# Performance work log

Measured on AMD Instinct MI355X. Metric: run time of the kernel, lower is better.

The kernel has to match this reference:

```python
import jax, jax.numpy as jnp
import numpy as np

D = 768      # d_model (hardcoded in module)
H = 12       # heads (ViT-Base)
HD = D // H  # head_dim = 64
FF = 4 * D   # mlp hidden = 3072
L = 32       # num_latents
B, N = 64, 197
EPS = 1e-6


def _ln(x, g, b):
    mu = jnp.mean(x, axis=-1, keepdims=True)
    var = jnp.mean(jnp.square(x - mu), axis=-1, keepdims=True)
    return (x - mu) * jax.lax.rsqrt(var + EPS) * g + b


def _attn_simple(q, k, v):
    # fusion attention: single-head, scale = C ** -0.5 over full dim
    C = q.shape[-1]
    a = jax.nn.softmax(jnp.einsum('bnc,bmc->bnm', q, k) * (C ** -0.5), axis=-1)
    return jnp.einsum('bnm,bmc->bnc', a, v)


def _mha(x, qkv_w, qkv_b, proj_w, proj_b):
    Bx, Nx, C = x.shape
    qkv = (x @ qkv_w + qkv_b).reshape(Bx, Nx, 3, H, HD)
    q, k, v = jnp.moveaxis(qkv, 2, 0)           # each [B, N, H, HD]
    scores = jnp.einsum('bnhd,bmhd->bhnm', q, k) * (HD ** -0.5)
    a = jax.nn.softmax(scores, axis=-1)
    out = jnp.einsum('bhnm,bmhd->bnhd', a, v).reshape(Bx, Nx, C)
    return out @ proj_w + proj_b


def _mlp(x, w1, b1, w2, b2):
    return jax.nn.gelu(x @ w1 + b1, approximate=False) @ w2 + b2


def setup_inputs() -> dict:
    key = jax.random.key(0)
    ks = iter(jax.random.split(key, 40))
    std = 0.02
    d = {
        'x': jax.random.normal(next(ks), (B, N, D), jnp.float32),
        'y': jax.random.normal(next(ks), (B, N, D), jnp.float32),
        'latents': jax.random.normal(next(ks), (1, L, D), jnp.float32) * std,
        'scale_a': jnp.zeros((1,), jnp.float32) + 0.1,
        'scale_v': jnp.zeros((1,), jnp.float32) + 0.1,
    }
    for p in ('p', 'm'):
        d[f'{p}_n1_g'] = jnp.ones((D,), jnp.float32)
        d[f'{p}_n1_b'] = jnp.zeros((D,), jnp.float32)
        d[f'{p}_qkv_w'] = jax.random.normal(next(ks), (D, 3 * D), jnp.float32) * std
        d[f'{p}_qkv_b'] = jnp.zeros((3 * D,), jnp.float32)
        d[f'{p}_proj_w'] = jax.random.normal(next(ks), (D, D), jnp.float32) * std
        d[f'{p}_proj_b'] = jnp.zeros((D,), jnp.float32)
        d[f'{p}_n2_g'] = jnp.ones((D,), jnp.float32)
        d[f'{p}_n2_b'] = jnp.zeros((D,), jnp.float32)
        d[f'{p}_fc1_w'] = jax.random.normal(next(ks), (D, FF), jnp.float32) * std
        d[f'{p}_fc1_b'] = jnp.zeros((FF,), jnp.float32)
        d[f'{p}_fc2_w'] = jax.random.normal(next(ks), (FF, D), jnp.float32) * std
        d[f'{p}_fc2_b'] = jnp.zeros((D,), jnp.float32)
    return d


def reference(x, y, latents, scale_a, scale_v,
              p_n1_g, p_n1_b, p_qkv_w, p_qkv_b, p_proj_w, p_proj_b,
              p_n2_g, p_n2_b, p_fc1_w, p_fc1_b, p_fc2_w, p_fc2_b,
              m_n1_g, m_n1_b, m_qkv_w, m_qkv_b, m_proj_w, m_proj_b,
              m_n2_g, m_n2_b, m_fc1_w, m_fc1_b, m_fc2_w, m_fc2_b):
    BS = x.shape[0]
    # ---- fusion: latent bottleneck cross-attention ----
    concat = jnp.concatenate([x, y], axis=1)                       # [B, 2N, D]
    lat = jnp.broadcast_to(latents, (BS, L, D))
    fused = _attn_simple(lat, concat, concat)                      # [B, L, D]
    x = x + scale_a * _attn_simple(x, fused, fused)
    y = y + scale_v * _attn_simple(y, fused, fused)
    # ---- pre-norm attn + MLP blocks ----
    x = x + _mha(_ln(x, p_n1_g, p_n1_b), p_qkv_w, p_qkv_b, p_proj_w, p_proj_b)
    y = y + _mha(_ln(y, m_n1_g, m_n1_b), m_qkv_w, m_qkv_b, m_proj_w, m_proj_b)
    x = x + _mlp(_ln(x, p_n2_g, p_n2_b), p_fc1_w, p_fc1_b, p_fc2_w, p_fc2_b)
    y = y + _mlp(_ln(y, m_n2_g, m_n2_b), m_fc1_w, m_fc1_b, m_fc2_w, m_fc2_b)
    return (x, y)
```

## Files before the change

kernel.cpp:

```cpp
#include <hip/hip_runtime.h>
#include <math.h>


namespace {

constexpr int BB = 64, NN = 197, DD = 768, HH = 12, HDIM = 64, FF = 3072, LL = 32;
constexpr int N2 = 2 * NN;
constexpr int ROWS = BB * NN;
constexpr float SCALE_D = 0.036084391824351615f;
constexpr float SCALE_H = 0.125f;

constexpr long long B_AHI    = 0;
constexpr long long B_ALO    = 19365888;
constexpr long long B_GHI    = 40894464;
constexpr long long B_GLO    = 118358016;
constexpr long long B_CONCAT = 0;
constexpr long long B_SCORES = 0;
constexpr long long B_QKV    = 125829120;
constexpr long long B_FUSED  = 242221056;
constexpr long long B_S1T    = 248512512;
constexpr long long B_A2     = 252706816;
constexpr long long B_S2     = 256901120;
constexpr long long B_PHI    = 258998272;
constexpr long long B_PLO    = 278364160;
constexpr long long B_WHI    = 297795584;
constexpr long long B_WLO    = 303038464;

__device__ inline ushort f2bf(float f) {
  unsigned x = __float_as_uint(f);
  unsigned r = (x + 0x7FFFu + ((x >> 16) & 1u)) >> 16;
  return (ushort)r;
}
__device__ inline float bf2f(ushort u) {
  return __uint_as_float(((unsigned)u) << 16);
}

using bf16x8v = __attribute__((ext_vector_type(8))) short;
using f32x4v  = __attribute__((ext_vector_type(4))) float;

enum { ME_BIAS = 0, ME_RESID_BIAS = 1, ME_GELU_SPLIT = 2 };

struct MP {
  const ushort* Ah; const ushort* Al; int lda;
  const ushort* Wh; const ushort* Wl; int ldw;
  float* C; int ldc;
  const float* bias;
  const float* R; int ldr;
  ushort* Oh; ushort* Ol; int ldo;
  int M, N, K;
  int nxb, nwg;
};

template <int EPI>
__global__ __launch_bounds__(256, 3) void mgemm_k(MP p) {
  __shared__ ushort sAh[128 * 32], sAl[128 * 32], sBh[128 * 32], sBl[128 * 32];
  const int tid = threadIdx.x;

  const int nwg = p.nwg;
  const int h = blockIdx.x;
  const int q = nwg >> 3, r = nwg & 7;
  const int xcd = h & 7, ii = h >> 3;
  const int wg = (xcd < r ? xcd * (q + 1) : r * (q + 1) + (xcd - r) * q) + ii;
  const int m0 = (wg / p.nxb) * 128;
  const int n0 = (wg % p.nxb) * 128;

  const int l = tid & 63, w = tid >> 6;
  const int wm = (w >> 1) * 64, wn = (w & 1) * 64;
  const int fr = l & 15, fq = l >> 4;

  ushort* const lbuf = (w == 0) ? sAh : (w == 1) ? sAl : (w == 2) ? sBh : sBl;
  const ushort* const gsrc = (w == 0) ? p.Ah : (w == 1) ? p.Al
                            : (w == 2) ? p.Wh : p.Wl;
  const int ldg   = (w < 2) ? p.lda : p.ldw;
  const int rbase = (w < 2) ? m0 : n0;
  const int rlim  = ((w < 2) ? p.M : p.N) - 1;
  const int rl = l >> 2;
  const int ch = l & 3;

  f32x4v acc[4][4];
#pragma unroll
  for (int i = 0; i < 4; ++i)
#pragma unroll
    for (int j = 0; j < 4; ++j)
#pragma unroll
      for (int t = 0; t < 4; ++t) acc[i][j][t] = 0.f;

  for (int k0 = 0; k0 < p.K; k0 += 32) {
#pragma unroll
    for (int j = 0; j < 8; ++j) {
      int rg = rbase + j * 16 + rl;
      rg = rg > rlim ? rlim : rg;
      const ushort* gp = gsrc + (long long)rg * ldg + k0 + ch * 8;
      __builtin_amdgcn_global_load_lds(
          (const __attribute__((address_space(1))) void*)gp,
          (__attribute__((address_space(3))) void*)(lbuf + j * 512),
          16, 0, 0);
    }
    __syncthreads();

    bf16x8v ah[4], al[4];
#pragma unroll
    for (int mi = 0; mi < 4; ++mi) {
      const int ro = (wm + mi * 16 + fr) * 32 + fq * 8;
      ah[mi] = *reinterpret_cast<const bf16x8v*>(&sAh[ro]);
      al[mi] = *reinterpret_cast<const bf16x8v*>(&sAl[ro]);
    }
#pragma unroll
    for (int ni = 0; ni < 4; ++ni) {
      const int ro = (wn + ni * 16 + fr) * 32 + fq * 8;
      const bf16x8v bh = *reinterpret_cast<const bf16x8v*>(&sBh[ro]);
      const bf16x8v bl = *reinterpret_cast<const bf16x8v*>(&sBl[ro]);
#pragma unroll
      for (int mi = 0; mi < 4; ++mi) {
        acc[mi][ni] = __builtin_amdgcn_mfma_f32_16x16x32_bf16(al[mi], bh, acc[mi][ni], 0, 0, 0);
        acc[mi][ni] = __builtin_amdgcn_mfma_f32_16x16x32_bf16(ah[mi], bl, acc[mi][ni], 0, 0, 0);
        acc[mi][ni] = __builtin_amdgcn_mfma_f32_16x16x32_bf16(ah[mi], bh, acc[mi][ni], 0, 0, 0);
      }
    }
    __syncthreads();
  }

#pragma unroll
  for (int mi = 0; mi < 4; ++mi) {
    const int rb = m0 + wm + mi * 16 + fq * 4;
#pragma unroll
    for (int ni = 0; ni < 4; ++ni) {
      const int col = n0 + wn + ni * 16 + fr;
#pragma unroll
      for (int t = 0; t < 4; ++t) {
        const int mg = rb + t;
        if (mg >= p.M) continue;
        float v = acc[mi][ni][t];
        if (EPI == ME_BIAS) {
          p.C[(long long)mg * p.ldc + col] = v + p.bias[col];
        } else if (EPI == ME_RESID_BIAS) {
          p.C[(long long)mg * p.ldc + col] =
              v + p.bias[col] + p.R[(long long)mg * p.ldr + col];
        } else {
          v += p.bias[col];
          v = 0.5f * v * (1.f + erff(v * 0.70710678118654752f));
          const ushort hh = f2bf(v);
          const long long o = (long long)mg * p.ldo + col;
          p.Oh[o] = hh;
          p.Ol[o] = f2bf(v - bf2f(hh));
        }
      }
    }
  }
}

template <int EPI>
static void launch_mgemm(hipStream_t st, MP p) {
  p.nxb = p.N / 128;
  p.nwg = p.nxb * ((p.M + 127) / 128);
  hipLaunchKernelGGL(HIP_KERNEL_NAME(mgemm_k<EPI>), dim3(p.nwg), dim3(256), 0, st, p);
}

struct GemmP {
  const float* A; long long sA1, sA2; int lda;
  const float* W; long long sW1, sW2; int ldw;
  float*       C; long long sC1, sC2; int ldc;
  const float* R; long long sR1, sR2; int ldr;
  const float* bias;
  const float* scaleptr;
  ushort* Oh; ushort* Ol;
  int M, N, K, Z2;
  float alpha;
};

enum { E_NONE = 0, E_BIAS = 1, E_RESID_SCALE = 4, E_SPLIT = 5 };

template <int BM, int BN, int BK, int TM, int TN, bool WT, int EPI>
__global__ __launch_bounds__(256) void gemm_k(GemmP p) {
  constexpr int NX = BN / TN;
  __shared__ float As[BK][BM + 4];
  __shared__ float Ws[BK][BN + 4];

  const int tid = threadIdx.x;
  const int z = blockIdx.z;
  const int z1 = z / p.Z2, z2 = z % p.Z2;
  const float* A = p.A + (long long)z1 * p.sA1 + (long long)z2 * p.sA2;
  const float* W = p.W + (long long)z1 * p.sW1 + (long long)z2 * p.sW2;
  float*       C = p.C ? p.C + (long long)z1 * p.sC1 + (long long)z2 * p.sC2 : nullptr;
  const float* R = p.R ? p.R + (long long)z1 * p.sR1 + (long long)z2 * p.sR2 : nullptr;
  ushort* Oh = p.Oh ? p.Oh + (long long)z1 * p.sC1 + (long long)z2 * p.sC2 : nullptr;
  ushort* Ol = p.Ol ? p.Ol + (long long)z1 * p.sC1 + (long long)z2 * p.sC2 : nullptr;

  const int m0 = blockIdx.y * BM;
  const int n0 = blockIdx.x * BN;
  const int tx = tid % NX;
  const int ty = tid / NX;

  float acc[TM][TN];
#pragma unroll
  for (int i = 0; i < TM; ++i)
#pragma unroll
    for (int j = 0; j < TN; ++j) acc[i][j] = 0.f;

  for (int k0 = 0; k0 < p.K; k0 += BK) {
    for (int l = tid; l < BM * BK; l += 256) {
      const int m = l / BK, kc = l % BK;
      const int mg = m0 + m, kg = k0 + kc;
      float v = 0.f;
      if (mg < p.M && kg < p.K) v = A[(long long)mg * p.lda + kg];
      As[kc][m] = v;
    }
    if (!WT) {
      for (int l = tid; l < BK * BN; l += 256) {
        const int kc = l / BN, n = l % BN;
        const int ng = n0 + n, kg = k0 + kc;
        float v = 0.f;
        if (ng < p.N && kg < p.K) v = W[(long long)kg * p.ldw + ng];
        Ws[kc][n] = v;
      }
    } else {
      for (int l = tid; l < BK * BN; l += 256) {
        const int n = l / BK, kc = l % BK;
        const int ng = n0 + n, kg = k0 + kc;
        float v = 0.f;
        if (ng < p.N && kg < p.K) v = W[(long long)ng * p.ldw + kg];
        Ws[kc][n] = v;
      }
    }
    __syncthreads();

#pragma unroll
    for (int kk = 0; kk < BK; ++kk) {
      float af[TM], wf[TN];
#pragma unroll
      for (int i = 0; i < TM; i += 4) {
        const float4 t = *reinterpret_cast<const float4*>(&As[kk][ty * TM + i]);
        af[i] = t.x; af[i + 1] = t.y; af[i + 2] = t.z; af[i + 3] = t.w;
      }
#pragma unroll
      for (int j = 0; j < TN; j += 4) {
        const float4 t = *reinterpret_cast<const float4*>(&Ws[kk][tx * TN + j]);
        wf[j] = t.x; wf[j + 1] = t.y; wf[j + 2] = t.z; wf[j + 3] = t.w;
      }
#pragma unroll
      for (int i = 0; i < TM; ++i)
#pragma unroll
        for (int j = 0; j < TN; ++j) acc[i][j] += af[i] * wf[j];
    }
    __syncthreads();
  }

  float sc = 0.f;
  if (EPI == E_RESID_SCALE) sc = p.scaleptr[0];
#pragma unroll
  for (int i = 0; i < TM; ++i) {
    const int mg = m0 + ty * TM + i;
    if (mg >= p.M) continue;
#pragma unroll
    for (int j = 0; j < TN; ++j) {
      const int ng = n0 + tx * TN + j;
      if (ng >= p.N) continue;
      float v = acc[i][j];
      if (EPI == E_NONE) v *= p.alpha;
      if (EPI == E_BIAS) v += p.bias[ng];
      if (EPI == E_RESID_SCALE) v = R[(long long)mg * p.ldr + ng] + sc * v;
      if (EPI == E_SPLIT) {
        const long long o = (long long)mg * p.ldc + ng;
        const ushort hh = f2bf(v);
        Oh[o] = hh;
        Ol[o] = f2bf(v - bf2f(hh));
      } else {
        C[(long long)mg * p.ldc + ng] = v;
      }
    }
  }
}

template <int BM, int BN, int BK, int TM, int TN, bool WT, int EPI>
static void launch_gemm(hipStream_t st, const GemmP& p, int Z) {
  dim3 grid((p.N + BN - 1) / BN, (p.M + BM - 1) / BM, Z);
  hipLaunchKernelGGL(HIP_KERNEL_NAME(gemm_k<BM, BN, BK, TM, TN, WT, EPI>),
                     grid, dim3(256), 0, st, p);
}


__global__ __launch_bounds__(256) void concat_k(const float* __restrict__ x,
                                                const float* __restrict__ y,
                                                float* __restrict__ c) {
  const long long total4 = (long long)BB * N2 * DD / 4;
  const long long i = (long long)blockIdx.x * 256 + threadIdx.x;
  if (i >= total4) return;
  const long long e = i * 4;
  const int b = (int)(e / ((long long)N2 * DD));
  const long long rem = e % ((long long)N2 * DD);
  const int r = (int)(rem / DD);
  const int col = (int)(rem % DD);
  const float* src = (r < NN) ? (x + ((long long)b * NN + r) * DD + col)
                              : (y + ((long long)b * NN + (r - NN)) * DD + col);
  reinterpret_cast<float4*>(c)[i] = *reinterpret_cast<const float4*>(src);
}

__global__ __launch_bounds__(256) void ln_split_k(const float* __restrict__ in,
                                                  ushort* __restrict__ oh,
                                                  ushort* __restrict__ ol,
                                                  const float* __restrict__ g,
                                                  const float* __restrict__ b) {
  const int row = blockIdx.x;
  const int tid = threadIdx.x;
  const float* src = in + (long long)row * DD;
  const float v0 = src[tid], v1 = src[tid + 256], v2 = src[tid + 512];
  __shared__ float red[4];
  const int wid = tid >> 6;

  float s = v0 + v1 + v2;
#pragma unroll
  for (int o = 32; o; o >>= 1) s += __shfl_xor(s, o);
  if ((tid & 63) == 0) red[wid] = s;
  __syncthreads();
  const float mu = (red[0] + red[1] + red[2] + red[3]) * (1.f / 768.f);
  const float d0 = v0 - mu, d1 = v1 - mu, d2 = v2 - mu;
  __syncthreads();

  float qv = d0 * d0 + d1 * d1 + d2 * d2;
#pragma unroll
  for (int o = 32; o; o >>= 1) qv += __shfl_xor(qv, o);
  if ((tid & 63) == 0) red[wid] = qv;
  __syncthreads();
  const float var = (red[0] + red[1] + red[2] + red[3]) * (1.f / 768.f);
  const float rs = 1.f / sqrtf(var + 1e-6f);

  ushort* dh = oh + (long long)row * DD;
  ushort* dl = ol + (long long)row * DD;
#pragma unroll
  for (int c = 0; c < 3; ++c) {
    const int idx = tid + c * 256;
    const float dv = (c == 0 ? d0 : c == 1 ? d1 : d2);
    const float v = dv * rs * g[idx] + b[idx];
    const ushort hh = f2bf(v);
    dh[idx] = hh;
    dl[idx] = f2bf(v - bf2f(hh));
  }
}

__global__ __launch_bounds__(256) void wsplit_k(const float* __restrict__ W,
                                                ushort* __restrict__ th,
                                                ushort* __restrict__ tl,
                                                int K, int N) {
  __shared__ float t[32][33];
  const int tid = threadIdx.x;
  const int kb = blockIdx.y * 32, nb = blockIdx.x * 32;
  for (int u = tid; u < 1024; u += 256) {
    const int k = u >> 5, n = u & 31;
    t[k][n] = W[(long long)(kb + k) * N + nb + n];
  }
  __syncthreads();
  const int n = tid >> 3, k4 = tid & 7;
  ushort4 vh, vl;
  {
    float v;
    v = t[k4 * 4 + 0][n]; vh.x = f2bf(v); vl.x = f2bf(v - bf2f(vh.x));
    v = t[k4 * 4 + 1][n]; vh.y = f2bf(v); vl.y = f2bf(v - bf2f(vh.y));
    v = t[k4 * 4 + 2][n]; vh.z = f2bf(v); vl.z = f2bf(v - bf2f(vh.z));
    v = t[k4 * 4 + 3][n]; vh.w = f2bf(v); vl.w = f2bf(v - bf2f(vh.w));
  }
  const long long o = (long long)(nb + n) * K + kb + k4 * 4;
  *reinterpret_cast<ushort4*>(th + o) = vh;
  *reinterpret_cast<ushort4*>(tl + o) = vl;
}

__global__ __launch_bounds__(256) void sm1_k(const float* __restrict__ S1t,
                                             float* __restrict__ A2) {
  const int b = blockIdx.x >> 5, l = blockIdx.x & 31;
  const int tid = threadIdx.x;
  const float* src = S1t + (long long)b * N2 * LL + l;
  const bool has2 = (tid + 256) < N2;
  const float v0 = src[(long long)tid * LL];
  const float v1 = has2 ? src[(long long)(tid + 256) * LL] : -3.0e38f;

  __shared__ float red[4];
  const int wid = tid >> 6;
  float mx = fmaxf(v0, v1);
#pragma unroll
  for (int o = 32; o; o >>= 1) mx = fmaxf(mx, __shfl_xor(mx, o));
  if ((tid & 63) == 0) red[wid] = mx;
  __syncthreads();
  mx = fmaxf(fmaxf(red[0], red[1]), fmaxf(red[2], red[3]));
  __syncthreads();

  const float p0 = expf(v0 - mx);
  const float p1 = has2 ? expf(v1 - mx) : 0.f;
  float s = p0 + p1;
#pragma unroll
  for (int o = 32; o; o >>= 1) s += __shfl_xor(s, o);
  if ((tid & 63) == 0) red[wid] = s;
  __syncthreads();
  const float inv = 1.f / (red[0] + red[1] + red[2] + red[3]);

  float* dst = A2 + (long long)b * LL * N2 + (long long)l * N2;
  dst[tid] = p0 * inv;
  if (has2) dst[tid + 256] = p1 * inv;
}

__global__ __launch_bounds__(256) void sm2_k(float* __restrict__ S, int rows) {
  const long long i = (long long)blockIdx.x * 256 + threadIdx.x;
  if (i >= rows) return;
  float* r = S + i * 32;
  float v[32];
  const float4* r4 = reinterpret_cast<const float4*>(r);
#pragma unroll
  for (int j = 0; j < 8; ++j) {
    const float4 t = r4[j];
    v[4 * j] = t.x; v[4 * j + 1] = t.y; v[4 * j + 2] = t.z; v[4 * j + 3] = t.w;
  }
  float mx = v[0];
#pragma unroll
  for (int j = 1; j < 32; ++j) mx = fmaxf(mx, v[j]);
  float s = 0.f;
#pragma unroll
  for (int j = 0; j < 32; ++j) { v[j] = expf(v[j] - mx); s += v[j]; }
  const float inv = 1.f / s;
  float4* w4 = reinterpret_cast<float4*>(r);
#pragma unroll
  for (int j = 0; j < 8; ++j) {
    float4 t;
    t.x = v[4 * j] * inv; t.y = v[4 * j + 1] * inv;
    t.z = v[4 * j + 2] * inv; t.w = v[4 * j + 3] * inv;
    w4[j] = t;
  }
}

__global__ __launch_bounds__(256) void smS_k(float* __restrict__ S, long long rows) {
  const int lane = threadIdx.x & 63;
  const long long row = (long long)blockIdx.x * 4 + (threadIdx.x >> 6);
  if (row >= rows) return;
  float* r = S + row * NN;
  float v[4];
#pragma unroll
  for (int j = 0; j < 4; ++j) {
    const int idx = lane + j * 64;
    v[j] = (idx < NN) ? r[idx] : -3.0e38f;
  }
  float mx = fmaxf(fmaxf(v[0], v[1]), fmaxf(v[2], v[3]));
#pragma unroll
  for (int o = 32; o; o >>= 1) mx = fmaxf(mx, __shfl_xor(mx, o));
  float pv[4];
  float s = 0.f;
#pragma unroll
  for (int j = 0; j < 4; ++j) {
    const int idx = lane + j * 64;
    pv[j] = (idx < NN) ? expf(v[j] - mx) : 0.f;
    s += pv[j];
  }
#pragma unroll
  for (int o = 32; o; o >>= 1) s += __shfl_xor(s, o);
  const float inv = 1.f / s;
#pragma unroll
  for (int j = 0; j < 4; ++j) {
    const int idx = lane + j * 64;
    if (idx < NN) r[idx] = pv[j] * inv;
  }
}

static GemmP mk(const float* A, long long sA1, long long sA2, int lda,
                const float* W, long long sW1, long long sW2, int ldw,
                float* C, long long sC1, long long sC2, int ldc,
                int M, int N, int K, int Z2, float alpha,
                const float* bias = nullptr,
                const float* R = nullptr, long long sR1 = 0, long long sR2 = 0, int ldr = 0,
                const float* scaleptr = nullptr) {
  GemmP p;
  p.A = A; p.sA1 = sA1; p.sA2 = sA2; p.lda = lda;
  p.W = W; p.sW1 = sW1; p.sW2 = sW2; p.ldw = ldw;
  p.C = C; p.sC1 = sC1; p.sC2 = sC2; p.ldc = ldc;
  p.R = R; p.sR1 = sR1; p.sR2 = sR2; p.ldr = ldr;
  p.bias = bias; p.scaleptr = scaleptr;
  p.Oh = nullptr; p.Ol = nullptr;
  p.M = M; p.N = N; p.K = K; p.Z2 = Z2; p.alpha = alpha;
  return p;
}

static MP mkm(const ushort* Ah, const ushort* Al, int lda,
              const ushort* Wh, const ushort* Wl, int ldw,
              int M, int N, int K, const float* bias,
              float* C = nullptr, int ldc = 0,
              const float* R = nullptr, int ldr = 0,
              ushort* Oh = nullptr, ushort* Ol = nullptr, int ldo = 0) {
  MP p;
  p.Ah = Ah; p.Al = Al; p.lda = lda;
  p.Wh = Wh; p.Wl = Wl; p.ldw = ldw;
  p.C = C; p.ldc = ldc; p.bias = bias;
  p.R = R; p.ldr = ldr;
  p.Oh = Oh; p.Ol = Ol; p.ldo = ldo;
  p.M = M; p.N = N; p.K = K;
  p.nxb = 0; p.nwg = 0;
  return p;
}

}

extern "C" void kernel_launch(void* const* d_in, const int* in_sizes, int n_in,
                              void* d_out, int out_size, void* d_ws, size_t ws_size,
                              hipStream_t stream) {
  const float* x   = (const float*)d_in[0];
  const float* y   = (const float*)d_in[1];
  const float* lat = (const float*)d_in[2];
  const float* scale_a = (const float*)d_in[3];
  const float* scale_v = (const float*)d_in[4];
  const float* PRM[2][12];
  for (int i = 0; i < 12; ++i) {
    PRM[0][i] = (const float*)d_in[5 + i];
    PRM[1][i] = (const float*)d_in[17 + i];
  }

  char* ws = (char*)d_ws;
  ushort* Ahi = (ushort*)(ws + B_AHI);
  ushort* Alo = (ushort*)(ws + B_ALO);
  ushort* Ghi = (ushort*)(ws + B_GHI);
  ushort* Glo = (ushort*)(ws + B_GLO);
  float* concat = (float*)(ws + B_CONCAT);
  float* scores = (float*)(ws + B_SCORES);
  float* qkv    = (float*)(ws + B_QKV);
  float* fused  = (float*)(ws + B_FUSED);
  float* S1t    = (float*)(ws + B_S1T);
  float* A2     = (float*)(ws + B_A2);
  float* S2     = (float*)(ws + B_S2);
  ushort* Phi   = (ushort*)(ws + B_PHI);
  ushort* Plo   = (ushort*)(ws + B_PLO);
  ushort* Whi   = (ushort*)(ws + B_WHI);
  ushort* Wlo   = (ushort*)(ws + B_WLO);

  float* outX = (float*)d_out;
  float* outY = outX + (long long)ROWS * DD;

  {
    const long long tot4 = (long long)BB * N2 * DD / 4;
    concat_k<<<(unsigned)((tot4 + 255) / 256), 256, 0, stream>>>(x, y, concat);
  }
  launch_gemm<128, 32, 8, 4, 4, true, E_NONE>(
      stream,
      mk(concat, (long long)N2 * DD, 0, DD,
         lat, 0, 0, DD,
         S1t, (long long)N2 * LL, 0, LL,
         N2, LL, DD, 1, SCALE_D),
      BB);
  sm1_k<<<BB * LL, 256, 0, stream>>>(S1t, A2);
  launch_gemm<32, 128, 8, 4, 4, false, E_NONE>(
      stream,
      mk(A2, (long long)LL * N2, 0, N2,
         concat, (long long)N2 * DD, 0, DD,
         fused, (long long)LL * DD, 0, DD,
         LL, DD, N2, 1, 1.f),
      BB);
  for (int s = 0; s < 2; ++s) {
    const float* qq = s == 0 ? x : y;
    const float* sp = s == 0 ? scale_a : scale_v;
    float* out = s == 0 ? outX : outY;
    launch_gemm<128, 32, 8, 4, 4, true, E_NONE>(
        stream,
        mk(qq, (long long)NN * DD, 0, DD,
           fused, (long long)LL * DD, 0, DD,
           S2, (long long)NN * LL, 0, LL,
           NN, LL, DD, 1, SCALE_D),
        BB);
    sm2_k<<<(BB * NN + 255) / 256, 256, 0, stream>>>(S2, BB * NN);
    launch_gemm<128, 128, 8, 8, 8, false, E_RESID_SCALE>(
        stream,
        mk(S2, (long long)NN * LL, 0, LL,
           fused, (long long)LL * DD, 0, DD,
           out, (long long)NN * DD, 0, DD,
           NN, DD, LL, 1, 1.f,
           nullptr,
           qq, (long long)NN * DD, 0, DD,
           sp),
        BB);
  }

  for (int s = 0; s < 2; ++s) {
    float* out = s == 0 ? outX : outY;
    const float* const* pp = PRM[s];
    const float *n1g = pp[0], *n1b = pp[1], *qkvw = pp[2], *qkvb = pp[3],
                *projw = pp[4], *projb = pp[5], *n2g = pp[6], *n2b = pp[7],
                *fc1w = pp[8], *fc1b = pp[9], *fc2w = pp[10], *fc2b = pp[11];

    ln_split_k<<<ROWS, 256, 0, stream>>>(out, Ahi, Alo, n1g, n1b);
    wsplit_k<<<dim3(3 * DD / 32, DD / 32), 256, 0, stream>>>(qkvw, Whi, Wlo, DD, 3 * DD);
    launch_mgemm<ME_BIAS>(stream,
        mkm(Ahi, Alo, DD, Whi, Wlo, DD, ROWS, 3 * DD, DD, qkvb, qkv, 3 * DD));
    launch_gemm<128, 128, 8, 8, 8, true, E_NONE>(
        stream,
        mk(qkv + 0 * DD, (long long)NN * 3 * DD, HDIM, 3 * DD,
           qkv + 1 * DD, (long long)NN * 3 * DD, HDIM, 3 * DD,
           scores, (long long)HH * NN * NN, (long long)NN * NN, NN,
           NN, NN, HDIM, HH, SCALE_H),
        BB * HH);
    smS_k<<<(unsigned)(((long long)BB * HH * NN + 3) / 4), 256, 0, stream>>>(
        scores, (long long)BB * HH * NN);
    {
      GemmP pv = mk(scores, (long long)HH * NN * NN, (long long)NN * NN, NN,
                    qkv + 2 * DD, (long long)NN * 3 * DD, HDIM, 3 * DD,
                    nullptr, (long long)NN * DD, HDIM, DD,
                    NN, HDIM, NN, HH, 1.f);
      pv.Oh = Phi; pv.Ol = Plo;
      launch_gemm<128, 64, 8, 8, 4, false, E_SPLIT>(stream, pv, BB * HH);
    }
    wsplit_k<<<dim3(DD / 32, DD / 32), 256, 0, stream>>>(projw, Whi, Wlo, DD, DD);
    launch_mgemm<ME_RESID_BIAS>(stream,
        mkm(Phi, Plo, DD, Whi, Wlo, DD, ROWS, DD, DD, projb, out, DD, out, DD));
    ln_split_k<<<ROWS, 256, 0, stream>>>(out, Ahi, Alo, n2g, n2b);
    wsplit_k<<<dim3(FF / 32, DD / 32), 256, 0, stream>>>(fc1w, Whi, Wlo, DD, FF);
    launch_mgemm<ME_GELU_SPLIT>(stream,
        mkm(Ahi, Alo, DD, Whi, Wlo, DD, ROWS, FF, DD, fc1b,
            nullptr, 0, nullptr, 0, Ghi, Glo, FF));
    wsplit_k<<<dim3(DD / 32, FF / 32), 256, 0, stream>>>(fc2w, Whi, Wlo, FF, DD);
    launch_mgemm<ME_RESID_BIAS>(stream,
        mkm(Ghi, Glo, FF, Whi, Wlo, FF, ROWS, DD, FF, fc2b, out, DD, out, DD));
  }
}
```

Measured before the change: 3.020 ms.

## Double-buffer split-bf16 GEMM LDS tiles and XOR-swizzle LDS layout

Adds double-buffered LDS staging to the split-bf16 MFMA GEMM, so the next K-slice's global-to-LDS loads are issued before computing on the current slice. This drops one barrier per iteration. It also XOR-swizzles the 16-byte chunk slot by row to reduce LDS bank conflicts on fragment reads. Shared memory doubles, and launch bounds drop from 3 to 2 waves per EU, which may cut occupancy.

Measured after the change: 3.108 ms. +2.9%, slower.

```diff
diff --git a/kernel.cpp b/kernel.cpp
--- a/kernel.cpp
+++ b/kernel.cpp
@@ -52,8 +52,8 @@
 };
 
 template <int EPI>
-__global__ __launch_bounds__(256, 3) void mgemm_k(MP p) {
-  __shared__ ushort sAh[128 * 32], sAl[128 * 32], sBh[128 * 32], sBl[128 * 32];
+__global__ __launch_bounds__(256, 2) void mgemm_k(MP p) {
+  __shared__ ushort lds[2 * 4 * 4096];
   const int tid = threadIdx.x;
 
   const int nwg = p.nwg;
@@ -68,14 +68,35 @@
   const int wm = (w >> 1) * 64, wn = (w & 1) * 64;
   const int fr = l & 15, fq = l >> 4;
 
-  ushort* const lbuf = (w == 0) ? sAh : (w == 1) ? sAl : (w == 2) ? sBh : sBl;
   const ushort* const gsrc = (w == 0) ? p.Ah : (w == 1) ? p.Al
                             : (w == 2) ? p.Wh : p.Wl;
   const int ldg   = (w < 2) ? p.lda : p.ldw;
   const int rbase = (w < 2) ? m0 : n0;
   const int rlim  = ((w < 2) ? p.M : p.N) - 1;
   const int rl = l >> 2;
-  const int ch = l & 3;
+  const int sl = l & 3;
+
+  int gcol[8], grow[8];
+#pragma unroll
+  for (int j = 0; j < 8; ++j) {
+    const int drow = j * 16 + rl;
+    const int lslot = sl ^ ((drow >> 1) & 3);
+    int rg = rbase + drow;
+    grow[j] = rg > rlim ? rlim : rg;
+    gcol[j] = lslot * 8;
+  }
+
+  int offA[4], offB[4];
+#pragma unroll
+  for (int mi = 0; mi < 4; ++mi) {
+    const int row = wm + mi * 16 + fr;
+    offA[mi] = row * 32 + (fq ^ ((row >> 1) & 3)) * 8;
+  }
+#pragma unroll
+  for (int ni = 0; ni < 4; ++ni) {
+    const int row = wn + ni * 16 + fr;
+    offB[ni] = row * 32 + (fq ^ ((row >> 1) & 3)) * 8;
+  }
 
   f32x4v acc[4][4];
 #pragma unroll
@@ -85,31 +106,47 @@
 #pragma unroll
       for (int t = 0; t < 4; ++t) acc[i][j][t] = 0.f;
 
-  for (int k0 = 0; k0 < p.K; k0 += 32) {
+  const int NK = p.K >> 5;
+
+  {
+    ushort* dst = &lds[w * 4096];
 #pragma unroll
     for (int j = 0; j < 8; ++j) {
-      int rg = rbase + j * 16 + rl;
-      rg = rg > rlim ? rlim : rg;
-      const ushort* gp = gsrc + (long long)rg * ldg + k0 + ch * 8;
+      const ushort* gp = gsrc + (long long)grow[j] * ldg + 0 + gcol[j];
       __builtin_amdgcn_global_load_lds(
           (const __attribute__((address_space(1))) void*)gp,
-          (__attribute__((address_space(3))) void*)(lbuf + j * 512),
+          (__attribute__((address_space(3))) void*)(dst + j * 512),
           16, 0, 0);
     }
-    __syncthreads();
-
+  }
+  __syncthreads();
+
+  int cur = 0;
+  for (int t = 0; t < NK; ++t) {
+    if (t + 1 < NK) {
+      const int k0 = (t + 1) << 5;
+      ushort* dst = &lds[((cur ^ 1) * 4 + w) * 4096];
+#pragma unroll
+      for (int j = 0; j < 8; ++j) {
+        const ushort* gp = gsrc + (long long)grow[j] * ldg + k0 + gcol[j];
+        __builtin_amdgcn_global_load_lds(
+            (const __attribute__((address_space(1))) void*)gp,
+            (__attribute__((address_space(3))) void*)(dst + j * 512),
+            16, 0, 0);
+      }
+    }
+
+    const int cb = cur * 16384;
     bf16x8v ah[4], al[4];
 #pragma unroll
     for (int mi = 0; mi < 4; ++mi) {
-      const int ro = (wm + mi * 16 + fr) * 32 + fq * 8;
-      ah[mi] = *reinterpret_cast<const bf16x8v*>(&sAh[ro]);
-      al[mi] = *reinterpret_cast<const bf16x8v*>(&sAl[ro]);
+      ah[mi] = *reinterpret_cast<const bf16x8v*>(&lds[cb + offA[mi]]);
+      al[mi] = *reinterpret_cast<const bf16x8v*>(&lds[cb + 4096 + offA[mi]]);
     }
 #pragma unroll
     for (int ni = 0; ni < 4; ++ni) {
-      const int ro = (wn + ni * 16 + fr) * 32 + fq * 8;
-      const bf16x8v bh = *reinterpret_cast<const bf16x8v*>(&sBh[ro]);
-      const bf16x8v bl = *reinterpret_cast<const bf16x8v*>(&sBl[ro]);
+      const bf16x8v bh = *reinterpret_cast<const bf16x8v*>(&lds[cb + 8192 + offB[ni]]);
+      const bf16x8v bl = *reinterpret_cast<const bf16x8v*>(&lds[cb + 12288 + offB[ni]]);
 #pragma unroll
       for (int mi = 0; mi < 4; ++mi) {
         acc[mi][ni] = __builtin_amdgcn_mfma_f32_16x16x32_bf16(al[mi], bh, acc[mi][ni], 0, 0, 0);
@@ -118,6 +155,7 @@
       }
     }
     __syncthreads();
+    cur ^= 1;
   }
 
 #pragma unroll
```
